# Optimization experiments

Hardware: AMD Instinct MI355X
Metric: run time of the kernel (lower is better)

## Reference

```python
import jax, jax.numpy as jnp
import numpy as np

NEG_INF = -1e16


def setup_inputs() -> dict:
    key = jax.random.key(0)
    k1, k2, k3 = jax.random.split(key, 3)
    B, N, C, D = 8, 4096, 64, 64
    inputs = jax.random.normal(k1, (B, N, C), dtype=jnp.float32)
    graph = jax.random.randint(k2, (N, N), 0, 2, dtype=jnp.int32)
    # xavier_uniform for Linear weight [D, C]
    limit = float(np.sqrt(6.0 / (C + D)))
    W = jax.random.uniform(k3, (D, C), dtype=jnp.float32, minval=-limit, maxval=limit)
    b = jnp.zeros((D,), dtype=jnp.float32)
    return {"inputs": inputs, "graph": graph, "W": W, "b": b}


def reference(inputs, graph, W, b):
    # h = W(inputs): [B, N, D]
    h = jnp.einsum('bnc,dc->bnd', inputs, W)
    # dense pairwise scores: [B, N, N]
    scores = jnp.einsum('bnd,bmd->bnm', h, h)
    # mask non-edges (graph broadcasts over batch)
    scores = jnp.where(graph[None, :, :] == 0, NEG_INF, scores)
    attention = jax.nn.softmax(scores, axis=2)
    out = jnp.einsum('bnm,bmd->bnd', attention, h) + b
    return out
```

## Files before the change

### kernel.cpp

```cpp
#include <hip/hip_runtime.h>
#include <stdint.h>

typedef _Float16 f16x8 __attribute__((ext_vector_type(8)));
typedef __fp16 half2_t __attribute__((ext_vector_type(2)));
typedef float f32x4 __attribute__((ext_vector_type(4)));

#define LOG2E 1.44269504088896340736f
#define NEGINF (-1e16f)

constexpr int kN = 4096;
constexpr int kD = 64;
constexpr int kB = 8;

__global__ __launch_bounds__(256) void hproj_kernel(const float* __restrict__ x,
                                                    const float* __restrict__ W,
                                                    _Float16* __restrict__ hout,
                                                    _Float16* __restrict__ hTout)
{
    __shared__ float Wt[64][64];
    __shared__ float xs[64][65];
    __shared__ _Float16 ht[64][68];

    const int tid = threadIdx.x;
    const int r   = tid >> 2;
    const int c0  = (tid & 3) * 16;

    #pragma unroll
    for (int j = 0; j < 16; j += 4) {
        const float4 v = *(const float4*)(W + r * 64 + c0 + j);
        Wt[c0 + j + 0][r] = v.x;
        Wt[c0 + j + 1][r] = v.y;
        Wt[c0 + j + 2][r] = v.z;
        Wt[c0 + j + 3][r] = v.w;
    }
    const long rowbase = (long)blockIdx.x * 64;
    #pragma unroll
    for (int j = 0; j < 16; j += 4) {
        const float4 v = *(const float4*)(x + (rowbase + r) * 64 + c0 + j);
        xs[r][c0 + j + 0] = v.x;
        xs[r][c0 + j + 1] = v.y;
        xs[r][c0 + j + 2] = v.z;
        xs[r][c0 + j + 3] = v.w;
    }
    __syncthreads();

    const int d0 = (tid & 3) * 16;
    f32x4 acc[4] = {{0.f,0.f,0.f,0.f},{0.f,0.f,0.f,0.f},{0.f,0.f,0.f,0.f},{0.f,0.f,0.f,0.f}};
    #pragma unroll 4
    for (int c = 0; c < 64; ++c) {
        const float xv = xs[r][c];
        const f32x4* wrow = (const f32x4*)&Wt[c][d0];
        #pragma unroll
        for (int k = 0; k < 4; ++k) acc[k] += wrow[k] * xv;
    }
    f16x8 o0, o1;
    #pragma unroll
    for (int j = 0; j < 8; ++j) {
        o0[j] = (_Float16)acc[j >> 2][j & 3];
        o1[j] = (_Float16)acc[2 + (j >> 2)][j & 3];
    }
    *(f16x8*)(hout + (rowbase + r) * 64 + d0)     = o0;
    *(f16x8*)(hout + (rowbase + r) * 64 + d0 + 8) = o1;

    #pragma unroll
    for (int j = 0; j < 8; ++j) {
        ht[r][d0 + j]     = o0[j];
        ht[r][d0 + 8 + j] = o1[j];
    }
    __syncthreads();

    const int bb = blockIdx.x >> 6;
    const int n0 = (int)(rowbase & (kN - 1));
    const int dr = tid >> 2;
    const int c4 = (tid & 3) * 16;
    f16x8 t0, t1;
    #pragma unroll
    for (int j = 0; j < 8; ++j) {
        t0[j] = ht[c4 + j][dr];
        t1[j] = ht[c4 + 8 + j][dr];
    }
    _Float16* dst = hTout + (long)bb * kD * kN + (long)dr * kN + n0 + c4;
    *(f16x8*)(dst)     = t0;
    *(f16x8*)(dst + 8) = t1;
}

__global__ __launch_bounds__(256) void bitpack_kernel(const int* __restrict__ g,
                                                      uint32_t* __restrict__ mw)
{
    const long w = (long)blockIdx.x * 256 + threadIdx.x;
    const int4* p = (const int4*)(g + w * 32);
    uint32_t bits = 0;
    #pragma unroll
    for (int j = 0; j < 8; ++j) {
        const int4 v = p[j];
        bits |= (uint32_t)(v.x != 0) << (j * 4 + 0);
        bits |= (uint32_t)(v.y != 0) << (j * 4 + 1);
        bits |= (uint32_t)(v.z != 0) << (j * 4 + 2);
        bits |= (uint32_t)(v.w != 0) << (j * 4 + 3);
    }
    mw[w] = bits;
}

__global__ __launch_bounds__(256) void masktr_kernel(const uint32_t* __restrict__ mw,
                                                     uint64_t* __restrict__ wmout)
{
    const int tid  = threadIdx.x;
    const int wv   = tid >> 6;
    const int lane = tid & 63;
    const int ll   = lane & 15;
    const int lg   = lane >> 4;
    const int pair = blockIdx.x * 4 + wv;
    const int q16  = pair >> 6;
    const int kv64 = pair & 63;

    const uint2 u = *(const uint2*)(mw + (long)(q16 * 16 + ll) * 128 + kv64 * 2);

    uint64_t Wb[16];
    #pragma unroll
    for (int s = 0; s < 16; ++s) {
        const int t = s >> 2, rr = s & 3;
        const uint32_t word = (t >= 2) ? u.y : u.x;
        const int pos = 8 * lg + 4 * (t & 1) + rr;
        Wb[s] = __ballot(((word >> pos) & 1u) != 0);
    }

    const int s = lane;
    uint64_t a0 = (s & 1) ? Wb[1]  : Wb[0];
    uint64_t a1 = (s & 1) ? Wb[3]  : Wb[2];
    uint64_t a2 = (s & 1) ? Wb[5]  : Wb[4];
    uint64_t a3 = (s & 1) ? Wb[7]  : Wb[6];
    uint64_t a4 = (s & 1) ? Wb[9]  : Wb[8];
    uint64_t a5 = (s & 1) ? Wb[11] : Wb[10];
    uint64_t a6 = (s & 1) ? Wb[13] : Wb[12];
    uint64_t a7 = (s & 1) ? Wb[15] : Wb[14];
    uint64_t b0 = (s & 2) ? a1 : a0;
    uint64_t b1 = (s & 2) ? a3 : a2;
    uint64_t b2 = (s & 2) ? a5 : a4;
    uint64_t b3 = (s & 2) ? a7 : a6;
    uint64_t c0 = (s & 4) ? b1 : b0;
    uint64_t c1 = (s & 4) ? b3 : b2;
    uint64_t v  = (s & 8) ? c1 : c0;
    if (lane < 16) wmout[(long)pair * 16 + lane] = v;
}

__global__ __launch_bounds__(512) void attn_kernel(const _Float16* __restrict__ h,
                                                   const _Float16* __restrict__ hT,
                                                   const uint64_t* __restrict__ wmask,
                                                   const float* __restrict__ bias,
                                                   float* __restrict__ outp,
                                                   float* __restrict__ pO,
                                                   float* __restrict__ pml,
                                                   int kvlen)
{
    __shared__ alignas(16) char Kl[2][8192];
    __shared__ alignas(16) char Vt[2][8192];

    const int b     = blockIdx.y;
    const int split = blockIdx.z;
    const int q0    = blockIdx.x * 128;
    const int tid   = threadIdx.x;
    const int wave  = tid >> 6;
    const int lane  = tid & 63;
    const int lg    = lane >> 4;
    const int ll    = lane & 15;

    const _Float16* hb  = h  + (long)b * kN * kD;
    const _Float16* hTb = hT + (long)b * kD * kN;
    const int kv_base = split * kvlen;
    const int NT      = kvlen / 64;

    const int q = q0 + wave * 16 + ll;
    const f16x8 qf0 = *(const f16x8*)(hb + q * 64 + lg * 8);
    const f16x8 qf1 = *(const f16x8*)(hb + q * 64 + 32 + lg * 8);

    f16x8 vone;
    {
        const _Float16 o = (ll == 0) ? (_Float16)1.0f : (_Float16)0.0f;
        #pragma unroll
        for (int j = 0; j < 8; ++j) vone[j] = o;
    }

    f32x4 Oacc[4] = {{0.f,0.f,0.f,0.f},{0.f,0.f,0.f,0.f},{0.f,0.f,0.f,0.f},{0.f,0.f,0.f,0.f}};
    f32x4 Oacc4 = {0.f, 0.f, 0.f, 0.f};
    float m_run = NEGINF;
    float mm = NEGINF * LOG2E;
    float negv = NEGINF;

    const int sr  = tid >> 3;
    const int sc8 = (tid & 7) * 8;
    const int srp = (sr & 0x23) | ((sr & 0x18) >> 1) | ((sr & 0x4) << 2);

    const int kw = srp * 128 + ((sc8 * 2) ^ ((srp & 7) << 4));
    const int vw = sr  * 128 + ((sc8 * 2) ^ ((sr  & 7) << 4));
    const int rb0 = ll * 128 + (((lg * 16))      ^ ((ll & 7) << 4));
    const int rb1 = ll * 128 + (((64 + lg * 16)) ^ ((ll & 7) << 4));

    char* const KB = (char*)Kl;
    char* const VB = (char*)Vt;

    const _Float16* gK = hb  + (long)(kv_base + sr) * 64 + sc8;
    const _Float16* gV = hTb + (long)sr * kN + kv_base + sc8;

    const int wuni = __builtin_amdgcn_readfirstlane(wave);
    const uint64_t* __restrict__ wmp =
        wmask + ((long)(blockIdx.x * 8 + wuni) * 64 + (kv_base >> 6)) * 16;

    uint64_t wmA[16], wmB[16];
    {
        const f16x8 a0 = *(const f16x8*)(gK);
        const f16x8 b0 = *(const f16x8*)(gV);
        *(f16x8*)(KB + kw) = a0;
        *(f16x8*)(VB + vw) = b0;
        gK += 64 * 64;  gV += 64;
        #pragma unroll
        for (int s = 0; s < 16; ++s) wmA[s] = wmp[s];
    }

#define TILE_BODY(WMC, WMN, IT, CB, NB)                                          \
    do {                                                                         \
        const int it_ = (IT);                                                    \
                  \
        f16x8 nk0{}, nv0{};                                                      \
        if (it_ + 1 < NT) {                                                      \
            nk0 = *(const f16x8*)(gK);                                           \
            nv0 = *(const f16x8*)(gV);                                           \
            gK += 64 * 64;  gV += 64;                                            \
        }                                                                        \
                    \
        asm volatile("s_waitcnt lgkmcnt(0)" ::: "memory");                       \
        __builtin_amdgcn_s_barrier();                                            \
        __builtin_amdgcn_sched_barrier(0);                                       \
                       \
        if (it_ + 1 < NT) {                                                      \
            _Pragma("unroll")                                                    \
            for (int s5 = 0; s5 < 16; ++s5) WMN[s5] = wmp[(long)(it_+1)*16 + s5];\
        }                                                                        \
        f32x4 S[4];                                                              \
        _Pragma("unroll")                                                        \
        for (int t = 0; t < 4; ++t) {                                            \
            const f16x8 k0 = *(const f16x8*)(KB + (CB) + rb0 + t * 2048);        \
            const f16x8 k1 = *(const f16x8*)(KB + (CB) + rb1 + t * 2048);        \
            f32x4 s = {0.f, 0.f, 0.f, 0.f};                                      \
            s = __builtin_amdgcn_mfma_f32_16x16x32_f16(k0, qf0, s, 0, 0, 0);     \
            s = __builtin_amdgcn_mfma_f32_16x16x32_f16(k1, qf1, s, 0, 0, 0);     \
            S[t] = s;                                                            \
        }                                                                        \
            \
                   \
        if (it_ + 1 < NT) {                                                      \
            *(f16x8*)(KB + (NB) + kw) = nk0;                                     \
            *(f16x8*)(VB + (NB) + vw) = nv0;                                     \
        }                                                                        \
        _Pragma("unroll")                                                        \
        for (int t = 0; t < 4; ++t) {                                            \
            _Pragma("unroll")                                                    \
            for (int rr = 0; rr < 4; ++rr) {                                     \
                float sv = S[t][rr];                                             \
                asm("v_cndmask_b32 %0, %1, %2, %3"                               \
                    : "=v"(sv) : "v"(negv), "v"(sv), "s"(WMC[t * 4 + rr]));      \
                S[t][rr] = sv;                                                   \
            }                                                                    \
        }                                                                        \
        float mx0 = fmaxf(fmaxf(S[0][0], S[0][1]), fmaxf(S[0][2], S[0][3]));     \
        float mx1 = fmaxf(fmaxf(S[1][0], S[1][1]), fmaxf(S[1][2], S[1][3]));     \
        float mx2 = fmaxf(fmaxf(S[2][0], S[2][1]), fmaxf(S[2][2], S[2][3]));     \
        float mx3 = fmaxf(fmaxf(S[3][0], S[3][1]), fmaxf(S[3][2], S[3][3]));     \
        float mloc = fmaxf(fmaxf(mx0, mx1), fmaxf(mx2, mx3));                    \
        mloc = fmaxf(mloc, __shfl_xor(mloc, 16));                                \
        mloc = fmaxf(mloc, __shfl_xor(mloc, 32));                                \
        if (__any(mloc > m_run + 8.f)) {                                         \
            const float mnew = fmaxf(m_run, mloc);                               \
            const float scl  = __builtin_amdgcn_exp2f((m_run - mnew) * LOG2E);   \
            m_run = mnew;                                                        \
            mm    = mnew * LOG2E;                                                \
            _Pragma("unroll")                                                    \
            for (int dt = 0; dt < 4; ++dt) Oacc[dt] *= scl;                      \
            Oacc4 *= scl;                                                        \
        }                                                                        \
        _Pragma("unroll")                                                        \
        for (int t = 0; t < 4; ++t) {                                            \
            _Pragma("unroll")                                                    \
            for (int rr = 0; rr < 4; ++rr)                                       \
                S[t][rr] = __builtin_amdgcn_exp2f(fmaf(S[t][rr], LOG2E, -mm));   \
        }                                                                        \
        union PF { half2_t hh[4]; f16x8 v; };                                    \
        PF pf1, pf2;                                                             \
        pf1.hh[0] = __builtin_amdgcn_cvt_pkrtz(S[0][0], S[0][1]);                \
        pf1.hh[1] = __builtin_amdgcn_cvt_pkrtz(S[0][2], S[0][3]);                \
        pf1.hh[2] = __builtin_amdgcn_cvt_pkrtz(S[1][0], S[1][1]);                \
        pf1.hh[3] = __builtin_amdgcn_cvt_pkrtz(S[1][2], S[1][3]);                \
        pf2.hh[0] = __builtin_amdgcn_cvt_pkrtz(S[2][0], S[2][1]);                \
        pf2.hh[1] = __builtin_amdgcn_cvt_pkrtz(S[2][2], S[2][3]);                \
        pf2.hh[2] = __builtin_amdgcn_cvt_pkrtz(S[3][0], S[3][1]);                \
        pf2.hh[3] = __builtin_amdgcn_cvt_pkrtz(S[3][2], S[3][3]);                \
        _Pragma("unroll")                                                        \
        for (int dt = 0; dt < 4; ++dt) {                                         \
            const f16x8 v0 = *(const f16x8*)(VB + (CB) + rb0 + dt * 2048);       \
            const f16x8 v1 = *(const f16x8*)(VB + (CB) + rb1 + dt * 2048);       \
            Oacc[dt] = __builtin_amdgcn_mfma_f32_16x16x32_f16(v0, pf1.v, Oacc[dt], 0, 0, 0); \
            Oacc[dt] = __builtin_amdgcn_mfma_f32_16x16x32_f16(v1, pf2.v, Oacc[dt], 0, 0, 0); \
        }                                                                        \
        Oacc4 = __builtin_amdgcn_mfma_f32_16x16x32_f16(vone, pf1.v, Oacc4, 0, 0, 0); \
        Oacc4 = __builtin_amdgcn_mfma_f32_16x16x32_f16(vone, pf2.v, Oacc4, 0, 0, 0); \
    } while (0)

    for (int ith = 0; ith < NT; ith += 2) {
        TILE_BODY(wmA, wmB, ith,     0,    8192);
        TILE_BODY(wmB, wmA, ith + 1, 8192, 0);
    }
#undef TILE_BODY

    const float lsum = __shfl(Oacc4[0], ll, 64);

    if (outp != nullptr) {
        const float inv = 1.0f / lsum;
        #pragma unroll
        for (int dt = 0; dt < 4; ++dt) {
            const int dbase = dt * 16 + lg * 4;
            const f32x4 bv = *(const f32x4*)(bias + dbase);
            f32x4 o;
            #pragma unroll
            for (int rr = 0; rr < 4; ++rr) o[rr] = Oacc[dt][rr] * inv + bv[rr];
            *(f32x4*)(outp + ((long)b * kN + q) * 64 + dbase) = o;
        }
    } else {
        const long srow = (long)split * kB * kN + (long)b * kN + q;
        #pragma unroll
        for (int dt = 0; dt < 4; ++dt) {
            const int dbase = dt * 16 + lg * 4;
            *(f32x4*)(pO + srow * 64 + dbase) = Oacc[dt];
        }
        if (lane < 16) {
            pml[srow * 2 + 0] = m_run;
            pml[srow * 2 + 1] = lsum;
        }
    }
}

__global__ __launch_bounds__(256) void combine_kernel(const float* __restrict__ pO,
                                                      const float* __restrict__ pml,
                                                      const float* __restrict__ bias,
                                                      float* __restrict__ outp,
                                                      int ks)
{
    const long idx = (long)blockIdx.x * 256 + threadIdx.x;
    const long row = idx >> 4;
    const int  d4  = (int)(idx & 15) * 4;

    float M = NEGINF;
    for (int s = 0; s < ks; ++s)
        M = fmaxf(M, pml[((long)s * kB * kN + row) * 2]);

    float L = 0.f;
    f32x4 acc = {0.f, 0.f, 0.f, 0.f};
    for (int s = 0; s < ks; ++s) {
        const long srow = (long)s * kB * kN + row;
        const float m = pml[srow * 2 + 0];
        const float l = pml[srow * 2 + 1];
        const float w = __builtin_amdgcn_exp2f((m - M) * LOG2E);
        L += l * w;
        const f32x4 o = *(const f32x4*)(pO + srow * 64 + d4);
        acc += o * w;
    }
    const float invL = (L > 0.f) ? (1.0f / L) : 0.f;
    const f32x4 bv = *(const f32x4*)(bias + d4);
    *(f32x4*)(outp + row * 64 + d4) = acc * invL + bv;
}

extern "C" void kernel_launch(void* const* d_in, const int* in_sizes, int n_in,
                              void* d_out, int out_size, void* d_ws, size_t ws_size,
                              hipStream_t stream) {
    const float*  x     = (const float*)d_in[0];
    const int*    graph = (const int*)d_in[1];
    const float*  W     = (const float*)d_in[2];
    const float*  bias  = (const float*)d_in[3];
    float*        outp  = (float*)d_out;

    char* ws = (char*)d_ws;
    _Float16* hptr  = (_Float16*)ws;
    uint32_t* mwptr = (uint32_t*)(ws + (4u << 20));
    _Float16* hTptr = (_Float16*)(ws + (6u << 20));
    uint64_t* wmptr = (uint64_t*)(ws + (10u << 20));

    int ks = 1;
    if      (ws_size >= ((size_t)46 << 20)) ks = 4;
    else if (ws_size >= ((size_t)30 << 20)) ks = 2;

    float* pO  = (float*)(ws + (12u << 20));
    float* pml = (float*)(ws + (12u << 20) + (size_t)ks * (8u << 20));

    hproj_kernel<<<dim3(kB * kN / 64), dim3(256), 0, stream>>>(x, W, hptr, hTptr);
    bitpack_kernel<<<dim3(kN * (kN / 32) / 256), dim3(256), 0, stream>>>(graph, mwptr);
    masktr_kernel<<<dim3(256 * 64 / 4), dim3(256), 0, stream>>>(mwptr, wmptr);

    if (ks == 1) {
        attn_kernel<<<dim3(kN / 128, kB, 1), dim3(512), 0, stream>>>(
            hptr, hTptr, wmptr, bias, outp, nullptr, nullptr, kN);
    } else {
        attn_kernel<<<dim3(kN / 128, kB, ks), dim3(512), 0, stream>>>(
            hptr, hTptr, wmptr, bias, nullptr, pO, pml, kN / ks);
        combine_kernel<<<dim3(kB * kN * 16 / 256), dim3(256), 0, stream>>>(
            pO, pml, bias, outp, ks);
    }
}
```

Baseline: 91.51 us.

## Store split-KV partials in fp16 and raise the split count

Partial attention outputs are normalized by their local sum and stored as fp16 instead of fp32, which halves partial-buffer traffic. The combine step now weights each normalized partial by l times the exponential correction. The smaller partials let the workspace hold more KV splits (up to 8), so more blocks run in parallel across the GPU. The cost is fp16 rounding on the partials and a heavier combine pass that reads more splits.

```diff
diff --git a/kernel.cpp b/kernel.cpp
--- a/kernel.cpp
+++ b/kernel.cpp
@@ -2,6 +2,7 @@
 #include <stdint.h>
 
 typedef _Float16 f16x8 __attribute__((ext_vector_type(8)));
+typedef _Float16 f16x4 __attribute__((ext_vector_type(4)));
 typedef __fp16 half2_t __attribute__((ext_vector_type(2)));
 typedef float f32x4 __attribute__((ext_vector_type(4)));
 
@@ -148,7 +149,7 @@
                                                    const uint64_t* __restrict__ wmask,
                                                    const float* __restrict__ bias,
                                                    float* __restrict__ outp,
-                                                   float* __restrict__ pO,
+                                                   _Float16* __restrict__ pO,
                                                    float* __restrict__ pml,
                                                    int kvlen)
 {
@@ -246,7 +247,6 @@
             S[t] = s;                                                            \
         }                                                                        \
             \
-                   \
         if (it_ + 1 < NT) {                                                      \
             *(f16x8*)(KB + (NB) + kw) = nk0;                                     \
             *(f16x8*)(VB + (NB) + vw) = nv0;                                     \
@@ -261,11 +261,12 @@
                 S[t][rr] = sv;                                                   \
             }                                                                    \
         }                                                                        \
-        float mx0 = fmaxf(fmaxf(S[0][0], S[0][1]), fmaxf(S[0][2], S[0][3]));     \
-        float mx1 = fmaxf(fmaxf(S[1][0], S[1][1]), fmaxf(S[1][2], S[1][3]));     \
-        float mx2 = fmaxf(fmaxf(S[2][0], S[2][1]), fmaxf(S[2][2], S[2][3]));     \
-        float mx3 = fmaxf(fmaxf(S[3][0], S[3][1]), fmaxf(S[3][2], S[3][3]));     \
-        float mloc = fmaxf(fmaxf(mx0, mx1), fmaxf(mx2, mx3));                    \
+                                \
+        float mx0 = fmaxf(fmaxf(fmaxf(S[0][0], S[0][1]), S[0][2]), S[0][3]);     \
+        float mx1 = fmaxf(fmaxf(fmaxf(S[1][0], S[1][1]), S[1][2]), S[1][3]);     \
+        float mx2 = fmaxf(fmaxf(fmaxf(S[2][0], S[2][1]), S[2][2]), S[2][3]);     \
+        float mx3 = fmaxf(fmaxf(fmaxf(S[3][0], S[3][1]), S[3][2]), S[3][3]);     \
+        float mloc = fmaxf(fmaxf(fmaxf(mx0, mx1), mx2), mx3);                    \
         mloc = fmaxf(mloc, __shfl_xor(mloc, 16));                                \
         mloc = fmaxf(mloc, __shfl_xor(mloc, 32));                                \
         if (__any(mloc > m_run + 8.f)) {                                         \
@@ -311,9 +312,9 @@
 #undef TILE_BODY
 
     const float lsum = __shfl(Oacc4[0], ll, 64);
+    const float inv  = (lsum > 0.f) ? (1.0f / lsum) : 0.f;
 
     if (outp != nullptr) {
-        const float inv = 1.0f / lsum;
         #pragma unroll
         for (int dt = 0; dt < 4; ++dt) {
             const int dbase = dt * 16 + lg * 4;
@@ -328,7 +329,10 @@
         #pragma unroll
         for (int dt = 0; dt < 4; ++dt) {
             const int dbase = dt * 16 + lg * 4;
-            *(f32x4*)(pO + srow * 64 + dbase) = Oacc[dt];
+            f16x4 po;
+            #pragma unroll
+            for (int rr = 0; rr < 4; ++rr) po[rr] = (_Float16)(Oacc[dt][rr] * inv);
+            *(f16x4*)(pO + srow * 64 + dbase) = po;
         }
         if (lane < 16) {
             pml[srow * 2 + 0] = m_run;
@@ -337,7 +341,7 @@
     }
 }
 
-__global__ __launch_bounds__(256) void combine_kernel(const float* __restrict__ pO,
+__global__ __launch_bounds__(256) void combine_kernel(const _Float16* __restrict__ pO,
                                                       const float* __restrict__ pml,
                                                       const float* __restrict__ bias,
                                                       float* __restrict__ outp,
@@ -357,10 +361,11 @@
         const long srow = (long)s * kB * kN + row;
         const float m = pml[srow * 2 + 0];
         const float l = pml[srow * 2 + 1];
-        const float w = __builtin_amdgcn_exp2f((m - M) * LOG2E);
-        L += l * w;
-        const f32x4 o = *(const f32x4*)(pO + srow * 64 + d4);
-        acc += o * w;
+        const float w = l * __builtin_amdgcn_exp2f((m - M) * LOG2E);
+        L += w;
+        const f16x4 o = *(const f16x4*)(pO + srow * 64 + d4);
+        #pragma unroll
+        for (int j = 0; j < 4; ++j) acc[j] += (float)o[j] * w;
     }
     const float invL = (L > 0.f) ? (1.0f / L) : 0.f;
     const f32x4 bv = *(const f32x4*)(bias + d4);
@@ -383,11 +388,12 @@
     uint64_t* wmptr = (uint64_t*)(ws + (10u << 20));
 
     int ks = 1;
-    if      (ws_size >= ((size_t)46 << 20)) ks = 4;
-    else if (ws_size >= ((size_t)30 << 20)) ks = 2;
-
-    float* pO  = (float*)(ws + (12u << 20));
-    float* pml = (float*)(ws + (12u << 20) + (size_t)ks * (8u << 20));
+    if      (ws_size >= ((size_t)47 << 20)) ks = 8;
+    else if (ws_size >= ((size_t)30 << 20)) ks = 4;
+    else if (ws_size >= ((size_t)21 << 20)) ks = 2;
+
+    _Float16* pO  = (_Float16*)(ws + (12u << 20));
+    float*    pml = (float*)(ws + (12u << 20) + (size_t)ks * (4u << 20));
 
     hproj_kernel<<<dim3(kB * kN / 64), dim3(256), 0, stream>>>(x, W, hptr, hTptr);
     bitpack_kernel<<<dim3(kN * (kN / 32) / 256), dim3(256), 0, stream>>>(graph, mwptr);
```

After: 93.78 us. 2.5% more time.
